# Optimization experiments

Measured on AMD Instinct MI355X. Metric: run time of the kernel, lower is better.

## Reference

```python
import jax, jax.numpy as jnp
import numpy as np

B, IN_C, OUT_C, K, Z_DIM = 32, 128, 128, 3, 512
H, W, STRIDE = 56, 56, 1


def setup_inputs() -> dict:
    key = jax.random.key(0)
    k1, k2, k3 = jax.random.split(key, 3)
    x = jax.random.normal(k1, (B, IN_C, H, W), dtype=jnp.float32)
    z = jax.random.normal(k2, (B, Z_DIM), dtype=jnp.float32)
    # nn.Linear(z_dim, out_c*in_c*k*k): weight [out_f, in_f], bias [out_f]
    out_f = OUT_C * IN_C * K * K
    W_head = jax.random.normal(k3, (out_f, Z_DIM), dtype=jnp.float32) * (1.0 / np.sqrt(Z_DIM))
    b_head = jnp.zeros((out_f,), dtype=jnp.float32)
    return {"x": x, "z": z, "W_head": W_head, "b_head": b_head}


def reference(x, z, W_head, b_head):
    b = x.shape[0]
    # hypernetwork head: per-sample conv weights
    w = z @ W_head.T + b_head                       # [B, out_c*in_c*k*k]
    w = w.reshape(b, OUT_C, IN_C, K, K)             # [B, O, I, K, K]

    pad = K // 2

    def conv_one(xi, wi):
        # xi: [I, H, W], wi: [O, I, K, K] -> [O, H', W']
        out = jax.lax.conv_general_dilated(
            xi[None],                                # [1, I, H, W]
            wi,
            window_strides=(STRIDE, STRIDE),
            padding=[(pad, pad), (pad, pad)],
            dimension_numbers=("NCHW", "OIHW", "NCHW"),
        )
        return out[0]

    return jax.vmap(conv_one)(x, w)                 # [B, O, H', W']
```

## Files before the change

kernel.cpp:

```cpp
#include <hip/hip_runtime.h>
#include <hip/hip_bf16.h>
#include <stdint.h>

#define BB 32
#define IC 128
#define OC 128
#define HH 56
#define WW 56
#define ZD 512
#define NRS 9
#define OI (OC*IC)
#define WROWS (OI*NRS)
#define NHEADBLK 1024
#define NTRBLK (HH * BB)
#define XP 58
#define XROW (XP * IC)
#define XBAT ((size_t)XP * XP * IC)

typedef float  f32x4  __attribute__((ext_vector_type(4)));
typedef short  bf16x8 __attribute__((ext_vector_type(8)));
typedef short  s16x4  __attribute__((ext_vector_type(4)));

static __device__ __forceinline__ short f2bf(float f) {
    uint32_t u = __float_as_uint(f);
    uint32_t r = (u + 0x7fffu + ((u >> 16) & 1u)) >> 16;
    return (short)r;
}
static __device__ __forceinline__ short f2bf_hw(float f) {
    __hip_bfloat16 h = __float2bfloat16(f);
    return *reinterpret_cast<short*>(&h);
}
static __device__ __forceinline__ float bf2f(short s) {
    uint32_t u = ((uint32_t)(uint16_t)s) << 16;
    return __uint_as_float(u);
}

__global__ __launch_bounds__(576, 1) void fused_head_tr_kernel(
    const float* __restrict__ Wh, const float* __restrict__ z,
    const float* __restrict__ bh, short* __restrict__ wbf,
    const float* __restrict__ x, short* __restrict__ xtp)
{
    if (blockIdx.x >= NHEADBLK) {
        const int bx = blockIdx.x - NHEADBLK;
        const int b = bx / HH;
        const int h = bx - b * HH;
        const int tid = threadIdx.x;
        short* xb = xtp + (size_t)b * XBAT;

        if (tid < 512) {
            const int w = tid & 63;
            const int yq = tid >> 6;
            if (w < WW) {
                const float* xp = x + (size_t)b * IC * HH * WW + h * WW + w;
                short* op = xb + ((size_t)(h + 1) * XP + (w + 1)) * IC;
                #pragma unroll
                for (int q = 0; q < 2; ++q) {
                    int ic = yq * 2 + q;
                    bf16x8 pk;
                    #pragma unroll
                    for (int j = 0; j < 8; ++j) {
                        float v = xp[(size_t)(ic * 8 + j) * (HH * WW)];
                        pk[j] = f2bf(v);
                    }
                    *(bf16x8*)(op + ic * 8) = pk;
                }
            }
        } else if (tid < 544) {
            int t = tid - 512;
            int u = (t >> 4) * (XP - 1);
            *(f32x4*)((char*)(xb + ((size_t)(h + 1) * XP + u) * IC) + (t & 15) * 16) =
                (f32x4){0.f, 0.f, 0.f, 0.f};
        }
        if (h == 0 || h == HH - 1) {
            const int v = (h == 0) ? 0 : XP - 1;
            char* rowp = (char*)(xb + (size_t)v * XROW);
            for (int idx = tid; idx < XROW * 2 / 16; idx += 576)
                *(f32x4*)(rowp + idx * 16) = (f32x4){0.f, 0.f, 0.f, 0.f};
        }
        return;
    }

    __shared__ __align__(16) char Zl[32 * 1024];
    __shared__ __align__(16) char Sl[144 * 64];
    const int tid  = threadIdx.x;
    const int lane = tid & 63;
    const int wv   = tid >> 6;

    if (tid < 256) {
        const int b = tid >> 3, ks = (tid & 7) * 64;
        const float* zp = z + (size_t)b * ZD + ks;
        const int bx = (b & 7) << 4;
        #pragma unroll
        for (int j8 = 0; j8 < 8; ++j8) {
            f32x4 v0 = *(const f32x4*)(zp + j8 * 8);
            f32x4 v1 = *(const f32x4*)(zp + j8 * 8 + 4);
            bf16x8 pk;
            pk[0] = f2bf_hw(v0.x); pk[1] = f2bf_hw(v0.y);
            pk[2] = f2bf_hw(v0.z); pk[3] = f2bf_hw(v0.w);
            pk[4] = f2bf_hw(v1.x); pk[5] = f2bf_hw(v1.y);
            pk[6] = f2bf_hw(v1.z); pk[7] = f2bf_hw(v1.w);
            *(bf16x8*)(Zl + b * 1024 + ((ks * 2 + j8 * 16) ^ bx)) = pk;
        }
    }
    __syncthreads();

    const int rl = lane & 15;
    const int kq = lane >> 4;
    const int zxor = (rl & 7) << 4;
    const int rowLocal = wv * 16 + rl;
    const int rowg = blockIdx.x * 144 + rowLocal;

    const char* wp = (const char*)Wh + (size_t)rowg * (ZD * 4) + kq * 32;

    f32x4 wd[16];
    #pragma unroll
    for (int i = 0; i < 8; ++i) {
        wd[2 * i]     = *(const f32x4*)(wp + i * 128);
        wd[2 * i + 1] = *(const f32x4*)(wp + i * 128 + 16);
    }

    f32x4 acc0 = {0.f, 0.f, 0.f, 0.f}, acc1 = {0.f, 0.f, 0.f, 0.f};
    #pragma unroll
    for (int kb = 0; kb < 16; ++kb) {
        const int sl = kb & 7;
        const int koff = (kb * 64 + kq * 16) ^ zxor;
        bf16x8 a0 = *(const bf16x8*)(Zl + rl * 1024 + koff);
        bf16x8 a1 = *(const bf16x8*)(Zl + (16 + rl) * 1024 + koff);
        f32x4 lo = wd[2 * sl];
        f32x4 hi = wd[2 * sl + 1];
        bf16x8 bw;
        bw[0] = f2bf_hw(lo.x); bw[1] = f2bf_hw(lo.y);
        bw[2] = f2bf_hw(lo.z); bw[3] = f2bf_hw(lo.w);
        bw[4] = f2bf_hw(hi.x); bw[5] = f2bf_hw(hi.y);
        bw[6] = f2bf_hw(hi.z); bw[7] = f2bf_hw(hi.w);
        acc0 = __builtin_amdgcn_mfma_f32_16x16x32_bf16(a0, bw, acc0, 0, 0, 0);
        acc1 = __builtin_amdgcn_mfma_f32_16x16x32_bf16(a1, bw, acc1, 0, 0, 0);
        if (kb < 8) {
            wd[2 * sl]     = *(const f32x4*)(wp + (kb + 8) * 128);
            wd[2 * sl + 1] = *(const f32x4*)(wp + (kb + 8) * 128 + 16);
        }
    }

    {
        const int swz = (rowLocal & 7) << 3;
        s16x4 s0, s1;
        #pragma unroll
        for (int reg = 0; reg < 4; ++reg) {
            s0[reg] = f2bf(acc0[reg]);
            s1[reg] = f2bf(acc1[reg]);
        }
        *(s16x4*)(Sl + rowLocal * 64 + ((kq * 8) ^ swz))      = s0;
        *(s16x4*)(Sl + rowLocal * 64 + ((32 + kq * 8) ^ swz)) = s1;
    }
    __syncthreads();

    if (tid < 512) {
        const int b  = tid >> 4;
        const int oiL = tid & 15;
        const int oi = blockIdx.x * 16 + oiL;
        #pragma unroll
        for (int rs = 0; rs < 9; ++rs) {
            const int rowL = oiL * 9 + rs;
            short sh = *(const short*)(Sl + rowL * 64 +
                                       ((2 * b) ^ ((rowL & 7) << 3)));
            float v = bf2f(sh) + bh[(size_t)oi * 9 + rs];
            wbf[((size_t)(b * 9 + rs)) * OI + oi] = f2bf(v);
        }
    }
}

__global__ __launch_bounds__(256) void conv_kernel(
    const short* __restrict__ wbf,
    const short* __restrict__ xtp,
    float* __restrict__ out)
{
    __shared__ __align__(16) char Wl[2][32768];
    const int tid  = threadIdx.x;
    const int lane = tid & 63;
    const int wv   = tid >> 6;
    const int og   = wv & 1;
    const int hh   = wv >> 1;

    const int bid = blockIdx.x;
    const int wg  = (bid & 7) * 112 + (bid >> 3);
    const int b   = wg / 28;
    const int h0  = (wg - b * 28) * 2;

    const short* xb = xtp + (size_t)b * XBAT;
    const int rl = lane & 15;
    const int kq = lane >> 4;

    f32x4 wr[8];
    #define WLOAD(rs_)                                                          \
        {                                                                       \
            const char* ws_ = (const char*)(wbf + ((size_t)b * NRS + (rs_)) * OI); \
            _Pragma("unroll")                                                   \
            for (int it_ = 0; it_ < 8; ++it_) {                                 \
                int c_ = (wv * 8 + it_) * 64 + lane;                            \
                int so_ = (c_ * 16) ^ (((c_ >> 4) & 7) << 4);                   \
                wr[it_] = *(const f32x4*)(ws_ + so_);                           \
            }                                                                   \
        }
    #define WSTORE(buf_)                                                        \
        _Pragma("unroll")                                                       \
        for (int it_ = 0; it_ < 8; ++it_)                                       \
            *(f32x4*)(Wl[buf_] + (wv * 8 + it_) * 1024 + lane * 16) = wr[it_];

    WLOAD(0);
    WSTORE(0);
    __syncthreads();
    WLOAD(1);

    f32x4 acc[4][4];
    #pragma unroll
    for (int a = 0; a < 4; ++a)
        #pragma unroll
        for (int p = 0; p < 4; ++p) acc[a][p] = (f32x4){0.f, 0.f, 0.f, 0.f};

    const int axor = (lane & 7) << 4;
    int kkoff[4];
    #pragma unroll
    for (int kk = 0; kk < 4; ++kk) kkoff[kk] = kk * 64 + (kq << 4);

    for (int rs = 0; rs < 9; ++rs) {
        const int r = rs / 3, s = rs - 3 * r;
        const char* Wb = Wl[rs & 1];
        const short* xrow = xb + (size_t)(h0 + hh + r) * XROW;
        int uoff[4];
        #pragma unroll
        for (int pf = 0; pf < 4; ++pf) {
            int p = pf * 16 + rl;
            int pc = p > 55 ? 55 : p;
            uoff[pf] = (pc + s) * IC + kq * 8;
        }
        #pragma unroll
        for (int kk = 0; kk < 4; ++kk) {
            bf16x8 av[4];
            #pragma unroll
            for (int af = 0; af < 4; ++af)
                av[af] = *(const bf16x8*)(Wb + (og * 64 + af * 16 + rl) * 256 +
                                          (kkoff[kk] ^ axor));
            #pragma unroll
            for (int pf = 0; pf < 4; ++pf) {
                bf16x8 bv = *(const bf16x8*)(xrow + uoff[pf] + kk * 32);
                #pragma unroll
                for (int af = 0; af < 4; ++af)
                    acc[af][pf] = __builtin_amdgcn_mfma_f32_16x16x32_bf16(
                        av[af], bv, acc[af][pf], 0, 0, 0);
            }
        }
        __syncthreads();
        if (rs < 8) { WSTORE((rs & 1) ^ 1); }
        if (rs < 7) { WLOAD(rs + 2); }
        __syncthreads();
    }
    #undef WLOAD
    #undef WSTORE

    const int hO = h0 + hh;
    #pragma unroll
    for (int af = 0; af < 4; ++af) {
        int o0 = og * 64 + af * 16 + kq * 4;
        #pragma unroll
        for (int pf = 0; pf < 4; ++pf) {
            int p = pf * 16 + rl;
            if (p < WW) {
                #pragma unroll
                for (int reg = 0; reg < 4; ++reg) {
                    out[(((size_t)b * OC + (o0 + reg)) * HH + hO) * WW + p] = acc[af][pf][reg];
                }
            }
        }
    }
}

extern "C" void kernel_launch(void* const* d_in, const int* in_sizes, int n_in,
                              void* d_out, int out_size, void* d_ws, size_t ws_size,
                              hipStream_t stream) {
    const float* x  = (const float*)d_in[0];
    const float* z  = (const float*)d_in[1];
    const float* Wh = (const float*)d_in[2];
    const float* bh = (const float*)d_in[3];
    float* out = (float*)d_out;

    short* wbf = (short*)d_ws;
    short* xtp = (short*)((char*)d_ws + 9437184);

    fused_head_tr_kernel<<<dim3(NHEADBLK + NTRBLK), 576, 0, stream>>>(Wh, z, bh, wbf, x, xtp);
    conv_kernel<<<dim3(28 * 32), 256, 0, stream>>>(wbf, xtp, out);
}
```

Measured before the change: 167.5 us.

## Stage input rows in LDS via direct global-to-LDS loads and widen conv tiles

The conv kernel now stages six padded input rows into LDS with global_load_lds and reads B operands from swizzled shared memory instead of global memory. Weight tiles are also loaded directly into LDS with async global_load_lds, using vmcnt waits and raw barriers in place of register staging. Each block now covers four output rows and all 128 output channels (8x4 accumulators per wave), which halves weight reloads per output. The grid shrinks to 448 blocks at one block per CU, and the larger register and LDS footprint risks lower occupancy.

```diff
diff --git a/kernel.cpp b/kernel.cpp
--- a/kernel.cpp
+++ b/kernel.cpp
@@ -16,6 +16,7 @@
 #define XP 58
 #define XROW (XP * IC)
 #define XBAT ((size_t)XP * XP * IC)
+#define WDIM 58
 
 typedef float  f32x4  __attribute__((ext_vector_type(4)));
 typedef short  bf16x8 __attribute__((ext_vector_type(8)));
@@ -33,6 +34,11 @@
 static __device__ __forceinline__ float bf2f(short s) {
     uint32_t u = ((uint32_t)(uint16_t)s) << 16;
     return __uint_as_float(u);
+}
+static __device__ __forceinline__ void gll16(const void* g, void* l) {
+    __builtin_amdgcn_global_load_lds(
+        (const __attribute__((address_space(1))) uint32_t*)g,
+        (__attribute__((address_space(3))) uint32_t*)l, 16, 0, 0);
 }
 
 __global__ __launch_bounds__(576, 1) void fused_head_tr_kernel(
@@ -169,51 +175,59 @@
     }
 }
 
-__global__ __launch_bounds__(256) void conv_kernel(
+__global__ __launch_bounds__(256, 1) void conv_kernel(
     const short* __restrict__ wbf,
     const short* __restrict__ xtp,
     float* __restrict__ out)
 {
+    __shared__ __align__(16) char Xl[6 * WDIM * 256];
     __shared__ __align__(16) char Wl[2][32768];
     const int tid  = threadIdx.x;
     const int lane = tid & 63;
     const int wv   = tid >> 6;
-    const int og   = wv & 1;
-    const int hh   = wv >> 1;
-
-    const int bid = blockIdx.x;
-    const int wg  = (bid & 7) * 112 + (bid >> 3);
-    const int b   = wg / 28;
-    const int h0  = (wg - b * 28) * 2;
-
-    const short* xb = xtp + (size_t)b * XBAT;
+    const int h0 = blockIdx.x * 4;
+    const int b  = blockIdx.y;
     const int rl = lane & 15;
     const int kq = lane >> 4;
 
-    f32x4 wr[8];
-    #define WLOAD(rs_)                                                          \
+    if (tid < 192) {
+        const int row = tid / 32;
+        const int cp  = (tid >> 4) & 1;
+        const int el  = tid & 15;
+        const int u   = row * WDIM + cp * (WDIM - 1);
+        *(f32x4*)(Xl + u * 256 + el * 16) = (f32x4){0.f, 0.f, 0.f, 0.f};
+    }
+    __syncthreads();
+
+    const short* xb = xtp + (size_t)b * XBAT;
+    for (int rr = 0; rr < 6; ++rr) {
+        const char* src = (const char*)(xb + (size_t)(h0 + rr) * XROW + IC);
+        char* dstb = Xl + (rr * WDIM + 1) * 256;
+        for (int it = wv; it < 14; it += 4) {
+            int c = it * 64 + lane;
+            int u = rr * WDIM + 1 + (c >> 4);
+            int soff = (c * 16) ^ ((u & 7) << 4);
+            gll16(src + soff, dstb + it * 1024);
+        }
+    }
+
+    #define STAGE_CW(rs_, buf_)                                                 \
         {                                                                       \
-            const char* ws_ = (const char*)(wbf + ((size_t)b * NRS + (rs_)) * OI); \
+            const char* ws_ = (const char*)(wbf +                               \
+                ((size_t)b * NRS + (rs_)) * OI);                                \
             _Pragma("unroll")                                                   \
             for (int it_ = 0; it_ < 8; ++it_) {                                 \
                 int c_ = (wv * 8 + it_) * 64 + lane;                            \
                 int so_ = (c_ * 16) ^ (((c_ >> 4) & 7) << 4);                   \
-                wr[it_] = *(const f32x4*)(ws_ + so_);                           \
+                gll16(ws_ + so_, Wl[buf_] + (wv * 8 + it_) * 1024);             \
             }                                                                   \
         }
-    #define WSTORE(buf_)                                                        \
-        _Pragma("unroll")                                                       \
-        for (int it_ = 0; it_ < 8; ++it_)                                       \
-            *(f32x4*)(Wl[buf_] + (wv * 8 + it_) * 1024 + lane * 16) = wr[it_];
-
-    WLOAD(0);
-    WSTORE(0);
-    __syncthreads();
-    WLOAD(1);
-
-    f32x4 acc[4][4];
-    #pragma unroll
-    for (int a = 0; a < 4; ++a)
+
+    STAGE_CW(0, 0);
+
+    f32x4 acc[8][4];
+    #pragma unroll
+    for (int a = 0; a < 8; ++a)
         #pragma unroll
         for (int p = 0; p < 4; ++p) acc[a][p] = (f32x4){0.f, 0.f, 0.f, 0.f};
 
@@ -223,44 +237,49 @@
     for (int kk = 0; kk < 4; ++kk) kkoff[kk] = kk * 64 + (kq << 4);
 
     for (int rs = 0; rs < 9; ++rs) {
+        __builtin_amdgcn_s_barrier();
+        __builtin_amdgcn_sched_barrier(0);
+        if (rs < 8) STAGE_CW(rs + 1, (rs + 1) & 1);
+        if (rs == 8) { asm volatile("s_waitcnt vmcnt(0)" ::: "memory"); }
+        else         { asm volatile("s_waitcnt vmcnt(8)" ::: "memory"); }
+        __builtin_amdgcn_sched_barrier(0);
+        __builtin_amdgcn_s_barrier();
+        __builtin_amdgcn_sched_barrier(0);
+
+        const char* Wb = Wl[rs & 1];
         const int r = rs / 3, s = rs - 3 * r;
-        const char* Wb = Wl[rs & 1];
-        const short* xrow = xb + (size_t)(h0 + hh + r) * XROW;
-        int uoff[4];
+        int ubase[4], bswz[4];
         #pragma unroll
         for (int pf = 0; pf < 4; ++pf) {
             int p = pf * 16 + rl;
             int pc = p > 55 ? 55 : p;
-            uoff[pf] = (pc + s) * IC + kq * 8;
+            int uu = (wv + r) * WDIM + pc + s;
+            ubase[pf] = uu * 256;
+            bswz[pf] = (uu & 7) << 4;
         }
         #pragma unroll
         for (int kk = 0; kk < 4; ++kk) {
-            bf16x8 av[4];
+            bf16x8 av[8];
             #pragma unroll
-            for (int af = 0; af < 4; ++af)
-                av[af] = *(const bf16x8*)(Wb + (og * 64 + af * 16 + rl) * 256 +
+            for (int af = 0; af < 8; ++af)
+                av[af] = *(const bf16x8*)(Wb + (af * 16 + rl) * 256 +
                                           (kkoff[kk] ^ axor));
             #pragma unroll
             for (int pf = 0; pf < 4; ++pf) {
-                bf16x8 bv = *(const bf16x8*)(xrow + uoff[pf] + kk * 32);
+                bf16x8 bv = *(const bf16x8*)(Xl + ubase[pf] + (kkoff[kk] ^ bswz[pf]));
                 #pragma unroll
-                for (int af = 0; af < 4; ++af)
+                for (int af = 0; af < 8; ++af)
                     acc[af][pf] = __builtin_amdgcn_mfma_f32_16x16x32_bf16(
                         av[af], bv, acc[af][pf], 0, 0, 0);
             }
         }
-        __syncthreads();
-        if (rs < 8) { WSTORE((rs & 1) ^ 1); }
-        if (rs < 7) { WLOAD(rs + 2); }
-        __syncthreads();
-    }
-    #undef WLOAD
-    #undef WSTORE
-
-    const int hO = h0 + hh;
-    #pragma unroll
-    for (int af = 0; af < 4; ++af) {
-        int o0 = og * 64 + af * 16 + kq * 4;
+    }
+    #undef STAGE_CW
+
+    const int hO = h0 + wv;
+    #pragma unroll
+    for (int af = 0; af < 8; ++af) {
+        int o0 = af * 16 + kq * 4;
         #pragma unroll
         for (int pf = 0; pf < 4; ++pf) {
             int p = pf * 16 + rl;
@@ -287,5 +306,5 @@
     short* xtp = (short*)((char*)d_ws + 9437184);
 
     fused_head_tr_kernel<<<dim3(NHEADBLK + NTRBLK), 576, 0, stream>>>(Wh, z, bh, wbf, x, xtp);
-    conv_kernel<<<dim3(28 * 32), 256, 0, stream>>>(wbf, xtp, out);
-}
+    conv_kernel<<<dim3(HH / 4, BB), 256, 0, stream>>>(wbf, xtp, out);
+}
```

Result: faster. 141.6 us (median of 2 runs) (-15.5%).
